# Kernel tuning notes

Measured on AMD Instinct MI355X. Metric: run time of the kernel, lower is better.

Reference implementation:

```python
import jax, jax.numpy as jnp
import numpy as np

# Module constants (from init_kwargs)
SEED_H = 32
SEED_W = 32
SEED_LEVEL = 4
EPS = 1e-8
OFFSETS = [(-1, -1), (-1, 0), (-1, 1), (0, -1), (0, 0), (0, 1), (1, -1), (1, 0), (1, 1)]


def setup_inputs() -> dict:
    key = jax.random.key(0)
    x = jax.random.normal(key, (8, 20, 512, 512), dtype=jnp.float32)
    return {"input": x}


def _seg_sum(vals, idx, num_segments):
    # vals: [B, HW] or [B, HW, C]; idx: [HW]
    return jax.vmap(lambda v: jax.ops.segment_sum(v, idx, num_segments=num_segments))(vals)


def _lattice_superpixel(x):
    B, C, H, W = x.shape
    ch, cw = H // SEED_H, W // SEED_W          # seed cell size
    S = SEED_H * SEED_W                        # number of seeds
    HW = H * W

    # initial seeds: mean of each lattice cell -> [B, C, SEED_H, SEED_W]
    seeds = x.reshape(B, C, SEED_H, ch, SEED_W, cw).mean(axis=(3, 5))

    # pixel -> candidate seed flat indices for the 3x3 seed neighborhood
    ph = jnp.arange(H) // ch                   # [H] seed row of each pixel
    pw = jnp.arange(W) // cw                   # [W] seed col of each pixel
    idxs = []
    for dy, dx in OFFSETS:
        iy = jnp.clip(ph + dy, 0, SEED_H - 1)
        ix = jnp.clip(pw + dx, 0, SEED_W - 1)
        idxs.append((iy[:, None] * SEED_W + ix[None, :]).reshape(-1))  # [HW]
    idxs = jnp.stack(idxs)                     # [9, HW]

    xp = x.transpose(0, 2, 3, 1).reshape(B, HW, C)  # pixel features [B, HW, C]

    Q = None
    for _ in range(SEED_LEVEL):
        # pixel-to-seed squared distances over the 9 candidate seeds
        sflat = seeds.reshape(B, C, S).transpose(0, 2, 1)  # [B, S, C]
        dists = []
        for o in range(9):
            s_o = sflat[:, idxs[o], :]                      # [B, HW, C]
            dists.append(jnp.sum((xp - s_o) ** 2, axis=-1))  # [B, HW]
        dist = jnp.stack(dists, axis=1)                     # [B, 9, HW]
        Q = jax.nn.softmax(-dist, axis=1)                   # soft associations

        # seed update: weighted mean of associated pixel features
        numer = jnp.zeros((B, S, C), x.dtype)
        denom = jnp.zeros((B, S), x.dtype)
        for o in range(9):
            w = Q[:, o, :]                                  # [B, HW]
            numer = numer + _seg_sum(w[..., None] * xp, idxs[o], S)
            denom = denom + _seg_sum(w, idxs[o], S)
        seeds = (numer / (denom[..., None] + EPS)).transpose(0, 2, 1).reshape(B, C, SEED_H, SEED_W)

    return Q.reshape(B, 9, H, W)


def reference(input) -> jnp.ndarray:
    return _lattice_superpixel(input)
```

## Files before the change

kernel.cpp:

```cpp
#include <hip/hip_runtime.h>

#define NB 8
#define NC 20
#define NH 512
#define NW 512
#define NS 1024
#define HW (NH * NW)
#define SEEDS_ELEMS (NB * NS * NC)
#define SNORM_ELEMS (NB * NS)
#define PART_STRIDE 189
#define EPSF 1e-8f

static constexpr int DYO[9] = {-1, -1, -1, 0, 0, 0, 1, 1, 1};
static constexpr int DXO[9] = {-1, 0, 1, -1, 0, 1, -1, 0, 1};

__device__ __forceinline__ int clampi(int v, int lo, int hi) {
    return v < lo ? lo : (v > hi ? hi : v);
}

__device__ __forceinline__ int xcd_cell(int bx) {
    return ((bx & 7) << 7) + (bx >> 3);
}

__global__ __launch_bounds__(160) void k_seed_init(const float* __restrict__ x,
                                                   float* __restrict__ seeds,
                                                   float* __restrict__ snorm) {
    __shared__ float sm[NC];
    const int tt = threadIdx.x;
    const int cell = blockIdx.x;
    const int b = blockIdx.y;
    const int cy = cell >> 5, cx = cell & 31;
    const int c = tt >> 3, s = tt & 7;

    const float* xb = x + (size_t)b * (NC * HW) + (size_t)c * HW
                        + (size_t)(cy << 4) * NW + (cx << 4);
    float acc = 0.f;
#pragma unroll
    for (int k = 0; k < 8; ++k) {
        const int row = (k << 1) + (s >> 2);
        const int col = (s & 3) << 2;
        const float4 v = *reinterpret_cast<const float4*>(xb + row * NW + col);
        acc += v.x + v.y + v.z + v.w;
    }
    acc += __shfl_xor(acc, 1, 64);
    acc += __shfl_xor(acc, 2, 64);
    acc += __shfl_xor(acc, 4, 64);
    if (s == 0) {
        const float mv = acc * (1.0f / 256.0f);
        seeds[((size_t)(b << 10) + cell) * NC + c] = mv;
        sm[c] = mv;
    }
    __syncthreads();
    if (tt == 0) {
        float n = 0.f;
#pragma unroll
        for (int cc = 0; cc < NC; ++cc) n += sm[cc] * sm[cc];
        snorm[(b << 10) + cell] = n;
    }
}

__global__ __launch_bounds__(256, 4) void k_iter(const float* __restrict__ x,
                                                 const float* __restrict__ seeds,
                                                 const float* __restrict__ snorm,
                                                 float* __restrict__ part) {
    __shared__ __align__(16) float qs[9 * 256];
    __shared__ float pbuf[4 * 9 * 24];

    const int t = threadIdx.x;
    const int cell = xcd_cell(blockIdx.x);
    const int b = blockIdx.y;
    const int cy = cell >> 5, cx = cell & 31;

    const float* xb = x + (size_t)b * (NC * HW) + (size_t)(cy << 4) * NW + (cx << 4);

    const float* xp = xb + (t >> 4) * NW + (t & 15);
    float xv[NC];
#pragma unroll
    for (int c = 0; c < NC; ++c) xv[c] = xp[(size_t)c * HW];

    float d[9];
#pragma unroll
    for (int o = 0; o < 9; ++o) {
        const int ny = clampi(cy + DYO[o], 0, 31);
        const int nx = clampi(cx + DXO[o], 0, 31);
        const int si = __builtin_amdgcn_readfirstlane((b << 10) + (ny << 5) + nx);
        const float* sp = seeds + (size_t)si * NC;
        float ip = 0.f;
#pragma unroll
        for (int c = 0; c < NC; ++c) ip += xv[c] * sp[c];
        d[o] = snorm[si] - 2.0f * ip;
    }
    float m = d[0];
#pragma unroll
    for (int o = 1; o < 9; ++o) m = fminf(m, d[o]);
    float w[9];
    float wsum = 0.f;
#pragma unroll
    for (int o = 0; o < 9; ++o) {
        w[o] = __expf(m - d[o]);
        wsum += w[o];
    }
    const float inv = 1.0f / wsum;
#pragma unroll
    for (int o = 0; o < 9; ++o) qs[(o << 8) + t] = w[o] * inv;
    __syncthreads();

    const int wid = t >> 6, tl = t & 63;
    if (tl < 56) {
        const int cg = tl >> 3, s = tl & 7;
        const int r0 = cg * 3;
        float acc[3][9];
#pragma unroll
        for (int j = 0; j < 3; ++j)
#pragma unroll
            for (int o = 0; o < 9; ++o) acc[j][o] = 0.f;

#pragma unroll
        for (int kk = 0; kk < 2; ++kk) {
            const int q = (((wid << 1) + kk) << 3) + s;
            const float* xr = xb + (q >> 2) * NW + ((q & 3) << 2);
            const float4 x0 = *reinterpret_cast<const float4*>(xr + (size_t)(r0 + 0) * HW);
            const float4 x1 = *reinterpret_cast<const float4*>(xr + (size_t)(r0 + 1) * HW);
            float4 x2 = make_float4(1.f, 1.f, 1.f, 1.f);
            if (cg < 6)
                x2 = *reinterpret_cast<const float4*>(xr + (size_t)(r0 + 2) * HW);
#pragma unroll
            for (int o = 0; o < 9; ++o) {
                const float4 q4 = *reinterpret_cast<const float4*>(&qs[(o << 8) + (q << 2)]);
                acc[0][o] += q4.x * x0.x + q4.y * x0.y + q4.z * x0.z + q4.w * x0.w;
                acc[1][o] += q4.x * x1.x + q4.y * x1.y + q4.z * x1.z + q4.w * x1.w;
                acc[2][o] += q4.x * x2.x + q4.y * x2.y + q4.z * x2.z + q4.w * x2.w;
            }
        }
#pragma unroll
        for (int j = 0; j < 3; ++j)
#pragma unroll
            for (int o = 0; o < 9; ++o) {
                acc[j][o] += __shfl_xor(acc[j][o], 1, 64);
                acc[j][o] += __shfl_xor(acc[j][o], 2, 64);
                acc[j][o] += __shfl_xor(acc[j][o], 4, 64);
            }
        if (s == 0) {
#pragma unroll
            for (int o = 0; o < 9; ++o)
#pragma unroll
                for (int j = 0; j < 3; ++j)
                    pbuf[wid * 216 + o * 24 + r0 + j] = acc[j][o];
        }
    }
    __syncthreads();

    if (t < PART_STRIDE) {
        const int o = t / 21, c = t - o * 21;
        const float v = pbuf[o * 24 + c] + pbuf[216 + o * 24 + c]
                      + pbuf[432 + o * 24 + c] + pbuf[648 + o * 24 + c];
        part[(size_t)((b << 10) + cell) * PART_STRIDE + t] = v;
    }
}

__global__ __launch_bounds__(192) void k_divz(const float* __restrict__ part,
                                              float* __restrict__ seeds,
                                              float* __restrict__ snorm) {
    __shared__ float den[8];
    __shared__ float sq[8][20];
    const int t = threadIdx.x;
    const int sl = t / 21, c = t - sl * 21;
    const int sid = blockIdx.x * 8 + sl;

    float tot = 0.f;
    if (t < 168) {
        const int b = sid >> 10;
        const int s1 = sid & 1023;
        const int sy = s1 >> 5, sx = s1 & 31;

        int cys[3], dys[3], cxs[3], dxs[3];
        cys[0] = sy > 0 ? sy - 1 : 0;   dys[0] = (sy == 0) ? -1 : 1;
        cys[1] = sy;                    dys[1] = 0;
        cys[2] = sy < 31 ? sy + 1 : 31; dys[2] = (sy == 31) ? 1 : -1;
        cxs[0] = sx > 0 ? sx - 1 : 0;   dxs[0] = (sx == 0) ? -1 : 1;
        cxs[1] = sx;                    dxs[1] = 0;
        cxs[2] = sx < 31 ? sx + 1 : 31; dxs[2] = (sx == 31) ? 1 : -1;

#pragma unroll
        for (int jy = 0; jy < 3; ++jy)
#pragma unroll
            for (int jx = 0; jx < 3; ++jx) {
                const int cell = (b << 10) + (cys[jy] << 5) + cxs[jx];
                const int o = (dys[jy] + 1) * 3 + (dxs[jx] + 1);
                tot += part[(size_t)cell * PART_STRIDE + o * 21 + c];
            }
        if (c == 20) den[sl] = tot;
    }
    __syncthreads();
    if (t < 168 && c < 20) {
        const float v = tot / (den[sl] + EPSF);
        seeds[(size_t)sid * NC + c] = v;
        sq[sl][c] = v * v;
    }
    __syncthreads();
    if (t < 8) {
        float n = 0.f;
#pragma unroll
        for (int cc = 0; cc < NC; ++cc) n += sq[t][cc];
        snorm[blockIdx.x * 8 + t] = n;
    }
}

__global__ __launch_bounds__(256, 4) void k_final(const float* __restrict__ x,
                                                  const float* __restrict__ seeds,
                                                  const float* __restrict__ snorm,
                                                  float* __restrict__ out) {
    const int t = threadIdx.x;
    const int cell = xcd_cell(blockIdx.x);
    const int b = blockIdx.y;
    const int cy = cell >> 5, cx = cell & 31;

    const int py = (cy << 4) + (t >> 4);
    const int px = (cx << 4) + (t & 15);
    const float* xp = x + (size_t)b * (NC * HW) + (size_t)py * NW + px;
    float xv[NC];
#pragma unroll
    for (int c = 0; c < NC; ++c) xv[c] = xp[(size_t)c * HW];

    float d[9];
#pragma unroll
    for (int o = 0; o < 9; ++o) {
        const int ny = clampi(cy + DYO[o], 0, 31);
        const int nx = clampi(cx + DXO[o], 0, 31);
        const int si = __builtin_amdgcn_readfirstlane((b << 10) + (ny << 5) + nx);
        const float* sp = seeds + (size_t)si * NC;
        float ip = 0.f;
#pragma unroll
        for (int c = 0; c < NC; ++c) ip += xv[c] * sp[c];
        d[o] = snorm[si] - 2.0f * ip;
    }
    float m = d[0];
#pragma unroll
    for (int o = 1; o < 9; ++o) m = fminf(m, d[o]);
    float w[9];
    float wsum = 0.f;
#pragma unroll
    for (int o = 0; o < 9; ++o) {
        w[o] = __expf(m - d[o]);
        wsum += w[o];
    }
    const float inv = 1.0f / wsum;
#pragma unroll
    for (int o = 0; o < 9; ++o) {
        out[(((size_t)b * 9 + o) * NH + py) * NW + px] = w[o] * inv;
    }
}

extern "C" void kernel_launch(void* const* d_in, const int* in_sizes, int n_in,
                              void* d_out, int out_size, void* d_ws, size_t ws_size,
                              hipStream_t stream) {
    const float* x = (const float*)d_in[0];
    float* out = (float*)d_out;

    float* seeds = (float*)d_ws;
    float* snorm = seeds + SEEDS_ELEMS;
    float* part  = snorm + SNORM_ELEMS;

    const dim3 grid(NS, NB);
    k_seed_init<<<grid, 160, 0, stream>>>(x, seeds, snorm);

    for (int it = 0; it < 3; ++it) {
        k_iter<<<grid, 256, 0, stream>>>(x, seeds, snorm, part);
        k_divz<<<NB * NS / 8, 192, 0, stream>>>(part, seeds, snorm);
    }
    k_final<<<grid, 256, 0, stream>>>(x, seeds, snorm, out);
}
```

Before: 447.9 us.

## Fuse seed division into iteration kernels and stage pixel tile in LDS

Removes the separate k_divz pass. Each k_iter and k_final block now rebuilds its 9 neighbour seeds directly from the previous partial sums and computes seed norms in-kernel, and partial buffers ping-pong between the workspace and the output buffer. The 20-channel pixel tile is loaded once into LDS with float4 loads and reused for both the distance and accumulation phases, instead of being read twice from global memory. The trade-off is redundant neighbour-partial gathers in every block, plus more LDS per block, which could limit occupancy.

Result: slower. 497.0 us (+11.0%).

```diff
diff --git a/kernel.cpp b/kernel.cpp
--- a/kernel.cpp
+++ b/kernel.cpp
@@ -7,8 +7,8 @@
 #define NS 1024
 #define HW (NH * NW)
 #define SEEDS_ELEMS (NB * NS * NC)
-#define SNORM_ELEMS (NB * NS)
 #define PART_STRIDE 189
+#define PART_ELEMS (NB * NS * PART_STRIDE)
 #define EPSF 1e-8f
 
 static constexpr int DYO[9] = {-1, -1, -1, 0, 0, 0, 1, 1, 1};
@@ -22,10 +22,31 @@
     return ((bx & 7) << 7) + (bx >> 3);
 }
 
+__device__ __forceinline__ float gather_seed(const float* __restrict__ part,
+                                             int b, int sy, int sx, int c) {
+    int cys[3], dys[3], cxs[3], dxs[3];
+    cys[0] = sy > 0 ? sy - 1 : 0;   dys[0] = (sy == 0) ? -1 : 1;
+    cys[1] = sy;                    dys[1] = 0;
+    cys[2] = sy < 31 ? sy + 1 : 31; dys[2] = (sy == 31) ? 1 : -1;
+    cxs[0] = sx > 0 ? sx - 1 : 0;   dxs[0] = (sx == 0) ? -1 : 1;
+    cxs[1] = sx;                    dxs[1] = 0;
+    cxs[2] = sx < 31 ? sx + 1 : 31; dxs[2] = (sx == 31) ? 1 : -1;
+    float totc = 0.f, totd = 0.f;
+#pragma unroll
+    for (int jy = 0; jy < 3; ++jy)
+#pragma unroll
+        for (int jx = 0; jx < 3; ++jx) {
+            const int gc = (b << 10) + (cys[jy] << 5) + cxs[jx];
+            const int oo = (dys[jy] + 1) * 3 + (dxs[jx] + 1);
+            const float* pp = part + (size_t)gc * PART_STRIDE + oo * 21;
+            totc += pp[c];
+            totd += pp[20];
+        }
+    return totc / (totd + EPSF);
+}
+
 __global__ __launch_bounds__(160) void k_seed_init(const float* __restrict__ x,
-                                                   float* __restrict__ seeds,
-                                                   float* __restrict__ snorm) {
-    __shared__ float sm[NC];
+                                                   float* __restrict__ seeds) {
     const int tt = threadIdx.x;
     const int cell = blockIdx.x;
     const int b = blockIdx.y;
@@ -45,25 +66,18 @@
     acc += __shfl_xor(acc, 1, 64);
     acc += __shfl_xor(acc, 2, 64);
     acc += __shfl_xor(acc, 4, 64);
-    if (s == 0) {
-        const float mv = acc * (1.0f / 256.0f);
-        seeds[((size_t)(b << 10) + cell) * NC + c] = mv;
-        sm[c] = mv;
-    }
-    __syncthreads();
-    if (tt == 0) {
-        float n = 0.f;
-#pragma unroll
-        for (int cc = 0; cc < NC; ++cc) n += sm[cc] * sm[cc];
-        snorm[(b << 10) + cell] = n;
-    }
+    if (s == 0)
+        seeds[((size_t)(b << 10) + cell) * NC + c] = acc * (1.0f / 256.0f);
 }
 
 __global__ __launch_bounds__(256, 4) void k_iter(const float* __restrict__ x,
-                                                 const float* __restrict__ seeds,
-                                                 const float* __restrict__ snorm,
-                                                 float* __restrict__ part) {
-    __shared__ __align__(16) float qs[9 * 256];
+                                                 const float* __restrict__ seeds0,
+                                                 const float* __restrict__ part_in,
+                                                 float* __restrict__ part_out,
+                                                 const int first) {
+    __shared__ __align__(16) float xs[NC][260];
+    __shared__ __align__(16) float qs[9][256];
+    __shared__ __align__(16) float s_seed[9][24];
     __shared__ float pbuf[4 * 9 * 24];
 
     const int t = threadIdx.x;
@@ -73,22 +87,44 @@
 
     const float* xb = x + (size_t)b * (NC * HW) + (size_t)(cy << 4) * NW + (cx << 4);
 
-    const float* xp = xb + (t >> 4) * NW + (t & 15);
+#pragma unroll
+    for (int j = 0; j < 5; ++j) {
+        const int Lq = (j << 8) + t;
+        const int c = Lq >> 6, qd = Lq & 63;
+        const float4 v = *reinterpret_cast<const float4*>(
+            xb + (size_t)c * HW + (qd >> 2) * NW + ((qd & 3) << 2));
+        *reinterpret_cast<float4*>(&xs[c][qd << 2]) = v;
+    }
+
+    if (t < 180) {
+        const int o = t / 20, c = t - o * 20;
+        const int sy = clampi(cy + DYO[o], 0, 31);
+        const int sx = clampi(cx + DXO[o], 0, 31);
+        float v;
+        if (first)
+            v = seeds0[((size_t)((b << 10) + (sy << 5) + sx)) * NC + c];
+        else
+            v = gather_seed(part_in, b, sy, sx, c);
+        s_seed[o][c] = v;
+    }
+    __syncthreads();
+
     float xv[NC];
 #pragma unroll
-    for (int c = 0; c < NC; ++c) xv[c] = xp[(size_t)c * HW];
+    for (int c = 0; c < NC; ++c) xv[c] = xs[c][t];
 
     float d[9];
 #pragma unroll
     for (int o = 0; o < 9; ++o) {
-        const int ny = clampi(cy + DYO[o], 0, 31);
-        const int nx = clampi(cx + DXO[o], 0, 31);
-        const int si = __builtin_amdgcn_readfirstlane((b << 10) + (ny << 5) + nx);
-        const float* sp = seeds + (size_t)si * NC;
-        float ip = 0.f;
-#pragma unroll
-        for (int c = 0; c < NC; ++c) ip += xv[c] * sp[c];
-        d[o] = snorm[si] - 2.0f * ip;
+        float ip = 0.f, sn = 0.f;
+#pragma unroll
+        for (int j = 0; j < 5; ++j) {
+            const float4 s4 = *reinterpret_cast<const float4*>(&s_seed[o][j << 2]);
+            ip += xv[(j << 2) + 0] * s4.x + xv[(j << 2) + 1] * s4.y
+                + xv[(j << 2) + 2] * s4.z + xv[(j << 2) + 3] * s4.w;
+            sn += s4.x * s4.x + s4.y * s4.y + s4.z * s4.z + s4.w * s4.w;
+        }
+        d[o] = sn - 2.0f * ip;
     }
     float m = d[0];
 #pragma unroll
@@ -102,7 +138,7 @@
     }
     const float inv = 1.0f / wsum;
 #pragma unroll
-    for (int o = 0; o < 9; ++o) qs[(o << 8) + t] = w[o] * inv;
+    for (int o = 0; o < 9; ++o) qs[o][t] = w[o] * inv;
     __syncthreads();
 
     const int wid = t >> 6, tl = t & 63;
@@ -118,15 +154,14 @@
 #pragma unroll
         for (int kk = 0; kk < 2; ++kk) {
             const int q = (((wid << 1) + kk) << 3) + s;
-            const float* xr = xb + (q >> 2) * NW + ((q & 3) << 2);
-            const float4 x0 = *reinterpret_cast<const float4*>(xr + (size_t)(r0 + 0) * HW);
-            const float4 x1 = *reinterpret_cast<const float4*>(xr + (size_t)(r0 + 1) * HW);
+            const float4 x0 = *reinterpret_cast<const float4*>(&xs[r0 + 0][q << 2]);
+            const float4 x1 = *reinterpret_cast<const float4*>(&xs[r0 + 1][q << 2]);
             float4 x2 = make_float4(1.f, 1.f, 1.f, 1.f);
             if (cg < 6)
-                x2 = *reinterpret_cast<const float4*>(xr + (size_t)(r0 + 2) * HW);
+                x2 = *reinterpret_cast<const float4*>(&xs[r0 + 2][q << 2]);
 #pragma unroll
             for (int o = 0; o < 9; ++o) {
-                const float4 q4 = *reinterpret_cast<const float4*>(&qs[(o << 8) + (q << 2)]);
+                const float4 q4 = *reinterpret_cast<const float4*>(&qs[o][q << 2]);
                 acc[0][o] += q4.x * x0.x + q4.y * x0.y + q4.z * x0.z + q4.w * x0.w;
                 acc[1][o] += q4.x * x1.x + q4.y * x1.y + q4.z * x1.z + q4.w * x1.w;
                 acc[2][o] += q4.x * x2.x + q4.y * x2.y + q4.z * x2.z + q4.w * x2.w;
@@ -154,62 +189,15 @@
         const int o = t / 21, c = t - o * 21;
         const float v = pbuf[o * 24 + c] + pbuf[216 + o * 24 + c]
                       + pbuf[432 + o * 24 + c] + pbuf[648 + o * 24 + c];
-        part[(size_t)((b << 10) + cell) * PART_STRIDE + t] = v;
-    }
-}
-
-__global__ __launch_bounds__(192) void k_divz(const float* __restrict__ part,
-                                              float* __restrict__ seeds,
-                                              float* __restrict__ snorm) {
-    __shared__ float den[8];
-    __shared__ float sq[8][20];
-    const int t = threadIdx.x;
-    const int sl = t / 21, c = t - sl * 21;
-    const int sid = blockIdx.x * 8 + sl;
-
-    float tot = 0.f;
-    if (t < 168) {
-        const int b = sid >> 10;
-        const int s1 = sid & 1023;
-        const int sy = s1 >> 5, sx = s1 & 31;
-
-        int cys[3], dys[3], cxs[3], dxs[3];
-        cys[0] = sy > 0 ? sy - 1 : 0;   dys[0] = (sy == 0) ? -1 : 1;
-        cys[1] = sy;                    dys[1] = 0;
-        cys[2] = sy < 31 ? sy + 1 : 31; dys[2] = (sy == 31) ? 1 : -1;
-        cxs[0] = sx > 0 ? sx - 1 : 0;   dxs[0] = (sx == 0) ? -1 : 1;
-        cxs[1] = sx;                    dxs[1] = 0;
-        cxs[2] = sx < 31 ? sx + 1 : 31; dxs[2] = (sx == 31) ? 1 : -1;
-
-#pragma unroll
-        for (int jy = 0; jy < 3; ++jy)
-#pragma unroll
-            for (int jx = 0; jx < 3; ++jx) {
-                const int cell = (b << 10) + (cys[jy] << 5) + cxs[jx];
-                const int o = (dys[jy] + 1) * 3 + (dxs[jx] + 1);
-                tot += part[(size_t)cell * PART_STRIDE + o * 21 + c];
-            }
-        if (c == 20) den[sl] = tot;
-    }
-    __syncthreads();
-    if (t < 168 && c < 20) {
-        const float v = tot / (den[sl] + EPSF);
-        seeds[(size_t)sid * NC + c] = v;
-        sq[sl][c] = v * v;
-    }
-    __syncthreads();
-    if (t < 8) {
-        float n = 0.f;
-#pragma unroll
-        for (int cc = 0; cc < NC; ++cc) n += sq[t][cc];
-        snorm[blockIdx.x * 8 + t] = n;
+        part_out[(size_t)((b << 10) + cell) * PART_STRIDE + t] = v;
     }
 }
 
 __global__ __launch_bounds__(256, 4) void k_final(const float* __restrict__ x,
-                                                  const float* __restrict__ seeds,
-                                                  const float* __restrict__ snorm,
+                                                  const float* __restrict__ part_in,
                                                   float* __restrict__ out) {
+    __shared__ __align__(16) float s_seed[9][24];
+
     const int t = threadIdx.x;
     const int cell = xcd_cell(blockIdx.x);
     const int b = blockIdx.y;
@@ -222,17 +210,26 @@
 #pragma unroll
     for (int c = 0; c < NC; ++c) xv[c] = xp[(size_t)c * HW];
 
+    if (t < 180) {
+        const int o = t / 20, c = t - o * 20;
+        const int sy = clampi(cy + DYO[o], 0, 31);
+        const int sx = clampi(cx + DXO[o], 0, 31);
+        s_seed[o][c] = gather_seed(part_in, b, sy, sx, c);
+    }
+    __syncthreads();
+
     float d[9];
 #pragma unroll
     for (int o = 0; o < 9; ++o) {
-        const int ny = clampi(cy + DYO[o], 0, 31);
-        const int nx = clampi(cx + DXO[o], 0, 31);
-        const int si = __builtin_amdgcn_readfirstlane((b << 10) + (ny << 5) + nx);
-        const float* sp = seeds + (size_t)si * NC;
-        float ip = 0.f;
-#pragma unroll
-        for (int c = 0; c < NC; ++c) ip += xv[c] * sp[c];
-        d[o] = snorm[si] - 2.0f * ip;
+        float ip = 0.f, sn = 0.f;
+#pragma unroll
+        for (int j = 0; j < 5; ++j) {
+            const float4 s4 = *reinterpret_cast<const float4*>(&s_seed[o][j << 2]);
+            ip += xv[(j << 2) + 0] * s4.x + xv[(j << 2) + 1] * s4.y
+                + xv[(j << 2) + 2] * s4.z + xv[(j << 2) + 3] * s4.w;
+            sn += s4.x * s4.x + s4.y * s4.y + s4.z * s4.z + s4.w * s4.w;
+        }
+        d[o] = sn - 2.0f * ip;
     }
     float m = d[0];
 #pragma unroll
@@ -258,15 +255,15 @@
     float* out = (float*)d_out;
 
     float* seeds = (float*)d_ws;
-    float* snorm = seeds + SEEDS_ELEMS;
-    float* part  = snorm + SNORM_ELEMS;
+    float* part0 = seeds + SEEDS_ELEMS;
+    float* part1 = (float*)d_out;
 
     const dim3 grid(NS, NB);
-    k_seed_init<<<grid, 160, 0, stream>>>(x, seeds, snorm);
-
-    for (int it = 0; it < 3; ++it) {
-        k_iter<<<grid, 256, 0, stream>>>(x, seeds, snorm, part);
-        k_divz<<<NB * NS / 8, 192, 0, stream>>>(part, seeds, snorm);
-    }
-    k_final<<<grid, 256, 0, stream>>>(x, seeds, snorm, out);
-}
+    k_seed_init<<<grid, 160, 0, stream>>>(x, seeds);
+
+    k_iter<<<grid, 256, 0, stream>>>(x, seeds, part0 , part0, 1);
+    k_iter<<<grid, 256, 0, stream>>>(x, seeds, part0, part1, 0);
+    k_iter<<<grid, 256, 0, stream>>>(x, seeds, part1, part0, 0);
+
+    k_final<<<grid, 256, 0, stream>>>(x, part0, out);
+}
```
